# Kernel optimization log

Measured on AMD Instinct MI355X. Metric: run time of the kernel, lower is better.

## Reference

```python
import jax, jax.numpy as jnp
import numpy as np

B, S, D, H = 4, 2048, 1024, 16
HD = D // H


def setup_inputs() -> dict:
    key = jax.random.key(0)
    k1, k2, k3 = jax.random.split(key, 3)
    scale = 1.0 / np.sqrt(D)
    return {
        "x": jax.random.normal(k1, (B, S, D), dtype=jnp.float32),
        "w_qkv": jax.random.normal(k2, (D, 3 * D), dtype=jnp.float32) * scale,
        "b_qkv": jnp.zeros((3 * D,), dtype=jnp.float32),
        "w_out": jax.random.normal(k3, (D, D), dtype=jnp.float32) * scale,
        "b_out": jnp.zeros((D,), dtype=jnp.float32),
    }


def reference(x, w_qkv, b_qkv, w_out, b_out):
    bsz, seqlen, embed = x.shape
    n_head = H
    head_dim = embed // n_head
    att_scale = 1.0 / np.sqrt(head_dim)

    qkv = x @ w_qkv + b_qkv                       # [b, s, 3d]
    q, k, v = jnp.split(qkv, 3, axis=2)
    # [b, h, s, hd]
    q = q.reshape(bsz, seqlen, n_head, head_dim).transpose(0, 2, 1, 3)
    k = k.reshape(bsz, seqlen, n_head, head_dim).transpose(0, 2, 1, 3)
    v = v.reshape(bsz, seqlen, n_head, head_dim).transpose(0, 2, 1, 3)

    att = jnp.einsum("bhqd,bhkd->bhqk", q, k) * att_scale
    causal = jnp.tril(jnp.ones((seqlen, seqlen), dtype=bool))
    att = jnp.where(causal, att, -jnp.inf)
    att = jax.nn.softmax(att, axis=-1)

    y = jnp.einsum("bhqk,bhkd->bhqd", att, v)     # [b, h, s, hd]
    y = y.transpose(0, 2, 1, 3).reshape(bsz, seqlen, embed)
    return y @ w_out + b_out
```

## Files before the change

kernel.cpp:

```cpp
#include <hip/hip_runtime.h>
#include <hip/hip_bf16.h>
#include <cmath>
#include <cstdint>

#define BB 4
#define SS 2048
#define DD 1024
#define HH 16
#define MM (BB * SS)

#define ATT_C 0.18033688011112042f

typedef __attribute__((ext_vector_type(8))) __bf16 bf16x8;
typedef __attribute__((ext_vector_type(4))) float f32x4;
typedef __attribute__((ext_vector_type(8))) float f32x8;
typedef __attribute__((ext_vector_type(8))) unsigned short u16x8;
typedef __attribute__((ext_vector_type(2))) unsigned int u32x2;
typedef __attribute__((ext_vector_type(4))) unsigned int u32x4;

typedef const __attribute__((address_space(3))) unsigned short* lds_cp;

__device__ __forceinline__ unsigned short f2bu(float f) {
  __hip_bfloat16 h = __float2bfloat16(f);
  return __builtin_bit_cast(unsigned short, h);
}

__device__ __forceinline__ f32x4 mfma16(bf16x8 a, bf16x8 b, f32x4 c) {
  return __builtin_amdgcn_mfma_f32_16x16x32_bf16(a, b, c, 0, 0, 0);
}

#define GLD16(gp, lp) __builtin_amdgcn_global_load_lds(                     \
    (const __attribute__((address_space(1))) void*)(gp),                    \
    (__attribute__((address_space(3))) void*)(lp), 16, 0, 0)

#define DSR128(dst, ptr, OFFLIT) \
  asm volatile("ds_read_b128 %0, %1 offset:" OFFLIT : "=v"(dst) : "v"(ptr))
#define LGKM(N) do { asm volatile("s_waitcnt lgkmcnt(" #N ")" ::: "memory"); \
                     __builtin_amdgcn_sched_barrier(0); } while (0)
#define VMCNT(N) do { asm volatile("s_waitcnt vmcnt(" #N ")" ::: "memory"); \
                      __builtin_amdgcn_sched_barrier(0); } while (0)

__global__ __launch_bounds__(256) void k_cast_bf16(const float* __restrict__ in,
                                                   unsigned short* __restrict__ out,
                                                   int n) {
  int i = (blockIdx.x * 256 + threadIdx.x) * 8;
  if (i >= n) return;
  f32x8 v = *(const f32x8*)(in + i);
  u16x8 o;
#pragma unroll
  for (int j = 0; j < 8; ++j) o[j] = f2bu(v[j]);
  *(u16x8*)(out + i) = o;
}

__global__ __launch_bounds__(256) void k_transpose_bf16(const float* __restrict__ in,
                                                        unsigned short* __restrict__ out,
                                                        int R, int C,
                                                        float scale, int scale_end) {
  __shared__ float tile[32][33];
  const int c0 = blockIdx.x * 32, r0 = blockIdx.y * 32;
  const int tx = threadIdx.x & 31, ty = threadIdx.x >> 5;
#pragma unroll
  for (int i = ty; i < 32; i += 8)
    tile[i][tx] = in[(size_t)(r0 + i) * C + c0 + tx];
  __syncthreads();
#pragma unroll
  for (int i = ty; i < 32; i += 8) {
    float v = tile[tx][i];
    if (c0 + i < scale_end) v *= scale;
    out[(size_t)(c0 + i) * R + r0 + tx] = f2bu(v);
  }
}

template <int OUT_F32>
__global__ __launch_bounds__(256) void k_gemm_bt(const unsigned short* __restrict__ A,
                                                 const unsigned short* __restrict__ Bt,
                                                 const float* __restrict__ bias,
                                                 void* __restrict__ Cout,
                                                 int M, int N, int K, int bias_scale_end) {
  __shared__ __attribute__((aligned(16))) unsigned short lA[2][128 * 64];
  __shared__ __attribute__((aligned(16))) unsigned short lB[2][128 * 64];
  const int tid = threadIdx.x;
  const int wave = tid >> 6, lane = tid & 63;
  const int g = lane >> 4, c = lane & 15;
  const int wr = wave >> 1, wc = wave & 1;
  const int m0 = blockIdx.y * 128, n0 = blockIdx.x * 128;
  const int srow = lane >> 3;
  const int sch  = ((lane & 7) ^ srow) * 8;

  f32x4 acc[4][4] = {};
  const int nkt = K >> 6;

#define GSTAGE(buf, kt) do {                                                     \
    const int k0s = (kt) * 64;                                                   \
    _Pragma("unroll")                                                            \
    for (int i_ = 0; i_ < 4; ++i_) {                                             \
      const int chunk = i_ * 4 + wave;                                           \
      GLD16(A + (size_t)(m0 + chunk * 8 + srow) * K + k0s + sch,                 \
            &lA[buf][0] + chunk * 512);                                          \
      GLD16(Bt + (size_t)(n0 + chunk * 8 + srow) * K + k0s + sch,                \
            &lB[buf][0] + chunk * 512);                                          \
    }                                                                            \
  } while (0)

  GSTAGE(0, 0);
  GSTAGE(1, 1);
  VMCNT(8);
  __syncthreads();

  int p = 0;
  for (int kt = 0; kt < nkt; ++kt) {
    const int x7 = c & 7;
    const lds_cp a0 = (lds_cp)&lA[p][0] + (wr * 64 + c) * 64 + (g ^ x7) * 8;
    const lds_cp b0 = (lds_cp)&lB[p][0] + (wc * 64 + c) * 64 + (g ^ x7) * 8;
    const lds_cp a1 = (lds_cp)&lA[p][0] + (wr * 64 + c) * 64 + ((g ^ x7) ^ 4) * 8;
    const lds_cp b1 = (lds_cp)&lB[p][0] + (wc * 64 + c) * 64 + ((g ^ x7) ^ 4) * 8;
    u32x4 af0[4], bf0[4], af1[4], bf1[4];
    DSR128(af0[0], a0, "0");    DSR128(af0[1], a0, "2048");
    DSR128(af0[2], a0, "4096"); DSR128(af0[3], a0, "6144");
    DSR128(bf0[0], b0, "0");    DSR128(bf0[1], b0, "2048");
    DSR128(bf0[2], b0, "4096"); DSR128(bf0[3], b0, "6144");
    DSR128(af1[0], a1, "0");    DSR128(af1[1], a1, "2048");
    DSR128(af1[2], a1, "4096"); DSR128(af1[3], a1, "6144");
    DSR128(bf1[0], b1, "0");    DSR128(bf1[1], b1, "2048");
    DSR128(bf1[2], b1, "4096"); DSR128(bf1[3], b1, "6144");

    LGKM(8);
    __builtin_amdgcn_s_setprio(1);
#pragma unroll
    for (int mi = 0; mi < 4; ++mi)
#pragma unroll
      for (int ni = 0; ni < 4; ++ni)
        acc[mi][ni] = mfma16(__builtin_bit_cast(bf16x8, af0[mi]),
                             __builtin_bit_cast(bf16x8, bf0[ni]), acc[mi][ni]);
    __builtin_amdgcn_s_setprio(0);

    LGKM(0);
    __syncthreads();
    if (kt + 2 < nkt) GSTAGE(p, kt + 2);

    __builtin_amdgcn_s_setprio(1);
#pragma unroll
    for (int mi = 0; mi < 4; ++mi)
#pragma unroll
      for (int ni = 0; ni < 4; ++ni)
        acc[mi][ni] = mfma16(__builtin_bit_cast(bf16x8, af1[mi]),
                             __builtin_bit_cast(bf16x8, bf1[ni]), acc[mi][ni]);
    __builtin_amdgcn_s_setprio(0);

    if (kt + 2 < nkt) { VMCNT(8); } else { VMCNT(0); }
    __syncthreads();
    p ^= 1;
  }
#undef GSTAGE

#pragma unroll
  for (int mi = 0; mi < 4; ++mi)
#pragma unroll
    for (int ni = 0; ni < 4; ++ni) {
      const int col = n0 + wc * 64 + ni * 16 + c;
      float bv = bias[col];
      if (col < bias_scale_end) bv *= ATT_C;
#pragma unroll
      for (int r = 0; r < 4; ++r) {
        const int row = m0 + wr * 64 + mi * 16 + g * 4 + r;
        const float v = acc[mi][ni][r] + bv;
        if (OUT_F32)
          ((float*)Cout)[(size_t)row * N + col] = v;
        else
          ((unsigned short*)Cout)[(size_t)row * N + col] = f2bu(v);
      }
    }
}

__global__ __launch_bounds__(256) void k_attn(const unsigned short* __restrict__ qkv,
                                              unsigned short* __restrict__ y) {
  __shared__ __attribute__((aligned(16))) unsigned short lK[2][4096];
  __shared__ __attribute__((aligned(16))) unsigned short lV[2][4096];

  const int tid = threadIdx.x, wave = tid >> 6, lane = tid & 63;
  const int g = lane >> 4, c = lane & 15;
  const int id = (int)blockIdx.x;
  const int xcd = id & 7, slot = id >> 3;
  const int bh = xcd + 8 * (slot & 7);
  const int pr = slot >> 3;
  const int b = bh >> 4, hc = bh & 15;
  const size_t rb = (size_t)b * SS;

  const int kRow = lane >> 3;
  const int kCh  = ((lane & 7) ^ kRow) * 8;
  const int vRow = 4 * ((lane >> 5) & 1) + ((lane >> 1) & 3);
  const int vDim = 16 * ((lane >> 3) & 3) + (lane & 1) * 8;

#define STAGE(buf, kb) do {                                                        \
    const int k0s = (kb) * 64;                                                     \
    const int g16 = wave * 16;                                                     \
    GLD16(qkv + (rb + k0s + g16 + kRow) * 3072 + 1024 + hc * 64 + kCh,             \
          &lK[buf][0] + g16 * 64);                                                 \
    GLD16(qkv + (rb + k0s + g16 + 8 + kRow) * 3072 + 1024 + hc * 64 + kCh,         \
          &lK[buf][0] + (g16 + 8) * 64);                                           \
    GLD16(qkv + (rb + k0s + g16 + vRow) * 3072 + 2048 + hc * 64 + vDim,            \
          &lV[buf][0] + g16 * 64);                                                 \
    GLD16(qkv + (rb + k0s + g16 + 8 + vRow) * 3072 + 2048 + hc * 64 + vDim,        \
          &lV[buf][0] + (g16 + 8) * 64);                                           \
  } while (0)

#define TRRD(dst, OFFLIT) \
  asm volatile("ds_read_b64_tr_b16 %0, %1 offset:" OFFLIT : "=v"(dst) : "v"(vp))

  bf16x8 onesf;
  {
    u16x8 t;
#pragma unroll
    for (int j = 0; j < 8; ++j) t[j] = 0x3F80;
    onesf = __builtin_bit_cast(bf16x8, t);
  }

  auto run_qtile = [&](int qt) {
    const int qw = qt * 128 + wave * 32;

    bf16x8 qf[2][2];
#pragma unroll
    for (int m = 0; m < 2; ++m)
#pragma unroll
      for (int kh = 0; kh < 2; ++kh)
        qf[m][kh] = *(const bf16x8*)(qkv + (rb + qw + m * 16 + c) * 3072 + hc * 64 + kh * 32 + g * 8);

    float mrun[2] = {-INFINITY, -INFINITY};
    f32x4 lsum[2] = {};
    f32x4 o[2][4] = {};
    const int nkb = 2 * qt + 2;

    auto compute = [&](int buf, int kb) {
      const int k0 = kb * 64;
      if (k0 > qw + 31) return;

      const lds_cp kbase = (lds_cp)&lK[buf][0];
      const lds_cp kp0 = kbase + c * 64 + ((g ^ (c & 7))) * 8;
      const lds_cp kp1 = kbase + c * 64 + (((4 + g) ^ (c & 7))) * 8;
      u32x4 kr[8];
      DSR128(kr[0], kp0, "0");    DSR128(kr[1], kp0, "2048");
      DSR128(kr[2], kp0, "4096"); DSR128(kr[3], kp0, "6144");
      DSR128(kr[4], kp1, "0");    DSR128(kr[5], kp1, "2048");
      DSR128(kr[6], kp1, "4096"); DSR128(kr[7], kp1, "6144");
      const lds_cp vp = (lds_cp)&lV[buf][0] + (lane >> 4) * 256 + (lane & 15) * 4;
      u32x2 t0[8];
      TRRD(t0[0], "0");   TRRD(t0[1], "2048");
      TRRD(t0[2], "128"); TRRD(t0[3], "2176");
      TRRD(t0[4], "256"); TRRD(t0[5], "2304");
      TRRD(t0[6], "384"); TRRD(t0[7], "2432");
      LGKM(8);

      f32x4 s[2][4];
      __builtin_amdgcn_s_setprio(1);
#pragma unroll
      for (int kf = 0; kf < 4; ++kf) {
        const bf16x8 ka = __builtin_bit_cast(bf16x8, kr[kf]);
        const bf16x8 kb2 = __builtin_bit_cast(bf16x8, kr[4 + kf]);
#pragma unroll
        for (int m = 0; m < 2; ++m) {
          f32x4 a = {};
          a = mfma16(ka, qf[m][0], a);
          a = mfma16(kb2, qf[m][1], a);
          s[m][kf] = a;
        }
      }
      __builtin_amdgcn_s_setprio(0);

      u32x2 t1[8];
      TRRD(t1[0], "4096"); TRRD(t1[1], "6144");
      TRRD(t1[2], "4224"); TRRD(t1[3], "6272");
      TRRD(t1[4], "4352"); TRRD(t1[5], "6400");
      TRRD(t1[6], "4480"); TRRD(t1[7], "6528");

#pragma unroll
      for (int m = 0; m < 2; ++m)
#pragma unroll
        for (int kf = 0; kf < 4; ++kf)
          if (k0 + kf * 16 + 15 > qw + m * 16) {
#pragma unroll
            for (int r = 0; r < 4; ++r)
              if (k0 + kf * 16 + 4 * g + r > qw + m * 16 + c) s[m][kf][r] = -INFINITY;
          }

#pragma unroll
      for (int m = 0; m < 2; ++m) {
        float a0 = fmaxf(fmaxf(s[m][0][0], s[m][0][1]), s[m][0][2]);
        float a1 = fmaxf(fmaxf(s[m][0][3], s[m][1][0]), s[m][1][1]);
        float a2 = fmaxf(fmaxf(s[m][1][2], s[m][1][3]), s[m][2][0]);
        float a3 = fmaxf(fmaxf(s[m][2][1], s[m][2][2]), s[m][2][3]);
        float a4 = fmaxf(fmaxf(s[m][3][0], s[m][3][1]), s[m][3][2]);
        float b0 = fmaxf(fmaxf(a0, a1), a2);
        float b1 = fmaxf(fmaxf(a3, a4), s[m][3][3]);
        float tmax = fmaxf(b0, b1);
        tmax = fmaxf(tmax, __shfl_xor(tmax, 16));
        tmax = fmaxf(tmax, __shfl_xor(tmax, 32));
        const float mold = mrun[m];
        float mt;
        if (__all(tmax - mold <= 8.f)) {
          mt = mold;
        } else {
          mt = fmaxf(mold, tmax);
          const float alpha = __builtin_amdgcn_exp2f(mold - mt);
          mrun[m] = mt;
#pragma unroll
          for (int r = 0; r < 4; ++r) {
            const float ao = __shfl(alpha, (lane & 48) + ((lane & 48) >> 2) + r);
            lsum[m][r] *= ao;
#pragma unroll
            for (int dc = 0; dc < 4; ++dc) o[m][dc][r] *= ao;
          }
        }
#pragma unroll
        for (int kf = 0; kf < 4; ++kf)
#pragma unroll
          for (int r = 0; r < 4; ++r)
            s[m][kf][r] = __builtin_amdgcn_exp2f(s[m][kf][r] - mt);
      }

      bf16x8 pa[2][2];
#pragma unroll
      for (int m = 0; m < 2; ++m)
#pragma unroll
        for (int kh = 0; kh < 2; ++kh) {
          u16x8 t;
#pragma unroll
          for (int j = 0; j < 4; ++j) {
            t[j]     = f2bu(s[m][2 * kh][j]);
            t[4 + j] = f2bu(s[m][2 * kh + 1][j]);
          }
          pa[m][kh] = __builtin_bit_cast(bf16x8, t);
        }

      LGKM(8);
      __builtin_amdgcn_s_setprio(1);
#pragma unroll
      for (int m = 0; m < 2; ++m) {
        lsum[m] = mfma16(pa[m][0], onesf, lsum[m]);
        lsum[m] = mfma16(pa[m][1], onesf, lsum[m]);
      }
#pragma unroll
      for (int dc = 0; dc < 4; ++dc) {
        u32x4 vv = {t0[2 * dc][0], t0[2 * dc][1], t0[2 * dc + 1][0], t0[2 * dc + 1][1]};
        const bf16x8 vf = __builtin_bit_cast(bf16x8, vv);
#pragma unroll
        for (int m = 0; m < 2; ++m) o[m][dc] = mfma16(pa[m][0], vf, o[m][dc]);
      }
      __builtin_amdgcn_s_setprio(0);

      LGKM(0);
      __builtin_amdgcn_s_setprio(1);
#pragma unroll
      for (int dc = 0; dc < 4; ++dc) {
        u32x4 vv = {t1[2 * dc][0], t1[2 * dc][1], t1[2 * dc + 1][0], t1[2 * dc + 1][1]};
        const bf16x8 vf = __builtin_bit_cast(bf16x8, vv);
#pragma unroll
        for (int m = 0; m < 2; ++m) o[m][dc] = mfma16(pa[m][1], vf, o[m][dc]);
      }
      __builtin_amdgcn_s_setprio(0);
    };

    __syncthreads();
    STAGE(0, 0);
    asm volatile("s_waitcnt vmcnt(0)" ::: "memory");
    __syncthreads();
    int cur = 0;
    for (int kb = 0; kb < nkb - 1; ++kb) {
      STAGE(cur ^ 1, kb + 1);
      compute(cur, kb);
      asm volatile("s_waitcnt vmcnt(0)" ::: "memory");
      __syncthreads();
      cur ^= 1;
    }
    compute(cur, nkb - 1);

#pragma unroll
    for (int m = 0; m < 2; ++m)
#pragma unroll
      for (int r = 0; r < 4; ++r) {
        const float inv = __builtin_amdgcn_rcpf(lsum[m][r]);
        const int q = qw + m * 16 + 4 * g + r;
#pragma unroll
        for (int dc = 0; dc < 4; ++dc)
          y[(rb + q) * 1024 + hc * 64 + dc * 16 + c] = f2bu(o[m][dc][r] * inv);
      }
  };

  run_qtile(15 - pr);
  run_qtile(pr);
#undef STAGE
#undef TRRD
}

extern "C" void kernel_launch(void* const* d_in, const int* in_sizes, int n_in,
                              void* d_out, int out_size, void* d_ws, size_t ws_size,
                              hipStream_t stream) {
  (void)in_sizes; (void)n_in; (void)out_size; (void)ws_size;
  const float* x     = (const float*)d_in[0];
  const float* w_qkv = (const float*)d_in[1];
  const float* b_qkv = (const float*)d_in[2];
  const float* w_out = (const float*)d_in[3];
  const float* b_out = (const float*)d_in[4];
  float* out = (float*)d_out;

  char* ws = (char*)d_ws;
  unsigned short* x_bf  = (unsigned short*)(ws);
  unsigned short* wqkvT = (unsigned short*)(ws + (size_t)16 * 1048576);
  unsigned short* woutT = (unsigned short*)(ws + (size_t)22 * 1048576);
  unsigned short* qkv   = (unsigned short*)(ws + (size_t)24 * 1048576);

  k_cast_bf16<<<dim3((MM * DD) / (256 * 8)), 256, 0, stream>>>(x, x_bf, MM * DD);
  k_transpose_bf16<<<dim3(3 * DD / 32, DD / 32), 256, 0, stream>>>(w_qkv, wqkvT, DD, 3 * DD,
                                                                   ATT_C, DD);
  k_transpose_bf16<<<dim3(DD / 32, DD / 32), 256, 0, stream>>>(w_out, woutT, DD, DD, 1.f, 0);

  k_gemm_bt<0><<<dim3(3 * DD / 128, MM / 128), 256, 0, stream>>>(
      x_bf, wqkvT, b_qkv, qkv, MM, 3 * DD, DD, DD);

  k_attn<<<dim3(512), 256, 0, stream>>>(qkv, x_bf);

  k_gemm_bt<1><<<dim3(DD / 128, MM / 128), 256, 0, stream>>>(
      x_bf, woutT, b_out, out, MM, DD, DD, 0);
}
```

Before: 173.3 us.

## Use 256x192 tile GEMM with 8 waves for QKV projection

```diff
diff --git a/kernel.cpp b/kernel.cpp
--- a/kernel.cpp
+++ b/kernel.cpp
@@ -39,6 +39,7 @@
                      __builtin_amdgcn_sched_barrier(0); } while (0)
 #define VMCNT(N) do { asm volatile("s_waitcnt vmcnt(" #N ")" ::: "memory"); \
                       __builtin_amdgcn_sched_barrier(0); } while (0)
+#define RBAR() __builtin_amdgcn_s_barrier()
 
 __global__ __launch_bounds__(256) void k_cast_bf16(const float* __restrict__ in,
                                                    unsigned short* __restrict__ out,
@@ -68,6 +69,127 @@
     float v = tile[tx][i];
     if (c0 + i < scale_end) v *= scale;
     out[(size_t)(c0 + i) * R + r0 + tx] = f2bu(v);
+  }
+}
+
+__global__ __launch_bounds__(512, 2) void k_gemm256(const unsigned short* __restrict__ A,
+                                                    const unsigned short* __restrict__ Bt,
+                                                    const float* __restrict__ bias,
+                                                    unsigned short* __restrict__ C,
+                                                    int M, int N, int K, int bse) {
+  __shared__ __attribute__((aligned(16))) unsigned short lA[2][256 * 64];
+  __shared__ __attribute__((aligned(16))) unsigned short lB[2][192 * 64];
+  const int tid = threadIdx.x;
+  const int wave = tid >> 6, lane = tid & 63;
+  const int g = lane >> 4, c = lane & 15;
+  const int wr = wave >> 2, wc = wave & 3;
+  const int m0 = blockIdx.y * 256, n0 = blockIdx.x * 192;
+  const int srow8 = tid >> 3;
+  const int sch = ((tid & 7) ^ (srow8 & 7)) * 8;
+
+  f32x4 acc[8][3] = {};
+  const int nkt = K >> 6;
+
+#define GST(buf, kt) do {                                                    \
+    const int k0s = (kt) * 64;                                               \
+    _Pragma("unroll")                                                        \
+    for (int j_ = 0; j_ < 4; ++j_)                                           \
+      GLD16(A + (size_t)(m0 + j_ * 64 + srow8) * K + k0s + sch,              \
+            &lA[buf][0] + (j_ * 64 + wave * 8) * 64);                        \
+    _Pragma("unroll")                                                        \
+    for (int j_ = 0; j_ < 3; ++j_)                                           \
+      GLD16(Bt + (size_t)(n0 + j_ * 64 + srow8) * K + k0s + sch,             \
+            &lB[buf][0] + (j_ * 64 + wave * 8) * 64);                        \
+  } while (0)
+
+  GST(0, 0);
+
+  for (int kt = 0; kt < nkt; ++kt) {
+    const int p = kt & 1;
+    if (kt + 1 < nkt) {
+      GST(p ^ 1, kt + 1);
+      VMCNT(7);
+    } else {
+      VMCNT(0);
+    }
+    RBAR();
+
+    const lds_cp ap = (lds_cp)&lA[p][0] + (wr * 128 + c) * 64;
+    const lds_cp bp = (lds_cp)&lB[p][0] + (wc * 48 + c) * 64;
+    const int x7 = c & 7;
+    const lds_cp ap0 = ap + (g ^ x7) * 8, ap1 = ap + ((4 + g) ^ x7) * 8;
+    const lds_cp bp0 = bp + (g ^ x7) * 8, bp1 = bp + ((4 + g) ^ x7) * 8;
+    u32x4 af[4], bf[3];
+
+    DSR128(af[0], ap0, "0");    DSR128(af[1], ap0, "2048");
+    DSR128(af[2], ap0, "4096"); DSR128(af[3], ap0, "6144");
+    DSR128(bf[0], bp0, "0");    DSR128(bf[1], bp0, "2048");  DSR128(bf[2], bp0, "4096");
+    RBAR(); LGKM(0);
+    __builtin_amdgcn_s_setprio(1);
+#pragma unroll
+    for (int mi = 0; mi < 4; ++mi)
+#pragma unroll
+      for (int ni = 0; ni < 3; ++ni)
+        acc[mi][ni] = mfma16(__builtin_bit_cast(bf16x8, af[mi]),
+                             __builtin_bit_cast(bf16x8, bf[ni]), acc[mi][ni]);
+    __builtin_amdgcn_s_setprio(0);
+    RBAR();
+
+    DSR128(af[0], ap0, "8192");  DSR128(af[1], ap0, "10240");
+    DSR128(af[2], ap0, "12288"); DSR128(af[3], ap0, "14336");
+    RBAR(); LGKM(0);
+    __builtin_amdgcn_s_setprio(1);
+#pragma unroll
+    for (int mi = 0; mi < 4; ++mi)
+#pragma unroll
+      for (int ni = 0; ni < 3; ++ni)
+        acc[4 + mi][ni] = mfma16(__builtin_bit_cast(bf16x8, af[mi]),
+                                 __builtin_bit_cast(bf16x8, bf[ni]), acc[4 + mi][ni]);
+    __builtin_amdgcn_s_setprio(0);
+    RBAR();
+
+    DSR128(af[0], ap1, "0");    DSR128(af[1], ap1, "2048");
+    DSR128(af[2], ap1, "4096"); DSR128(af[3], ap1, "6144");
+    DSR128(bf[0], bp1, "0");    DSR128(bf[1], bp1, "2048");  DSR128(bf[2], bp1, "4096");
+    RBAR(); LGKM(0);
+    __builtin_amdgcn_s_setprio(1);
+#pragma unroll
+    for (int mi = 0; mi < 4; ++mi)
+#pragma unroll
+      for (int ni = 0; ni < 3; ++ni)
+        acc[mi][ni] = mfma16(__builtin_bit_cast(bf16x8, af[mi]),
+                             __builtin_bit_cast(bf16x8, bf[ni]), acc[mi][ni]);
+    __builtin_amdgcn_s_setprio(0);
+    RBAR();
+
+    DSR128(af[0], ap1, "8192");  DSR128(af[1], ap1, "10240");
+    DSR128(af[2], ap1, "12288"); DSR128(af[3], ap1, "14336");
+    RBAR(); LGKM(0);
+    __builtin_amdgcn_s_setprio(1);
+#pragma unroll
+    for (int mi = 0; mi < 4; ++mi)
+#pragma unroll
+      for (int ni = 0; ni < 3; ++ni)
+        acc[4 + mi][ni] = mfma16(__builtin_bit_cast(bf16x8, af[mi]),
+                                 __builtin_bit_cast(bf16x8, bf[ni]), acc[4 + mi][ni]);
+    __builtin_amdgcn_s_setprio(0);
+    RBAR();
+  }
+#undef GST
+
+#pragma unroll
+  for (int ni = 0; ni < 3; ++ni) {
+    const int col = n0 + wc * 48 + ni * 16 + c;
+    float bv = bias[col];
+    if (col < bse) bv *= ATT_C;
+#pragma unroll
+    for (int mi = 0; mi < 8; ++mi) {
+#pragma unroll
+      for (int r = 0; r < 4; ++r) {
+        const int row = m0 + wr * 128 + mi * 16 + g * 4 + r;
+        C[(size_t)row * N + col] = f2bu(acc[mi][ni][r] + bv);
+      }
+    }
   }
 }
 
@@ -413,7 +535,7 @@
                                                                    ATT_C, DD);
   k_transpose_bf16<<<dim3(DD / 32, DD / 32), 256, 0, stream>>>(w_out, woutT, DD, DD, 1.f, 0);
 
-  k_gemm_bt<0><<<dim3(3 * DD / 128, MM / 128), 256, 0, stream>>>(
+  k_gemm256<<<dim3(3 * DD / 192, MM / 256), 512, 0, stream>>>(
       x_bf, wqkvT, b_qkv, qkv, MM, 3 * DD, DD, DD);
 
   k_attn<<<dim3(512), 256, 0, stream>>>(qkv, x_bf);
```

New measurement: 175.4 us. No clear change (+1.2%).

## Split attention KV loop across two wave groups and merge partial softmax states

Applied to the files above, without the earlier changes.

```diff
diff --git a/kernel.cpp b/kernel.cpp
--- a/kernel.cpp
+++ b/kernel.cpp
@@ -172,12 +172,12 @@
     }
 }
 
-__global__ __launch_bounds__(256) void k_attn(const unsigned short* __restrict__ qkv,
+__global__ __launch_bounds__(512) void k_attn(const unsigned short* __restrict__ qkv,
                                               unsigned short* __restrict__ y) {
-  __shared__ __attribute__((aligned(16))) unsigned short lK[2][4096];
-  __shared__ __attribute__((aligned(16))) unsigned short lV[2][4096];
+  __shared__ __attribute__((aligned(16))) unsigned short smem[32768];
 
   const int tid = threadIdx.x, wave = tid >> 6, lane = tid & 63;
+  const int grp = wave >> 2, gw = wave & 3;
   const int g = lane >> 4, c = lane & 15;
   const int id = (int)blockIdx.x;
   const int xcd = id & 7, slot = id >> 3;
@@ -191,17 +191,22 @@
   const int vRow = 4 * ((lane >> 5) & 1) + ((lane >> 1) & 3);
   const int vDim = 16 * ((lane >> 3) & 3) + (lane & 1) * 8;
 
-#define STAGE(buf, kb) do {                                                        \
+#define KBASE(par) (&smem[0] + (grp * 2 + (par)) * 4096)
+#define VBASE(par) (&smem[16384] + (grp * 2 + (par)) * 4096)
+
+#define STAGE(par, kb) do {                                                        \
     const int k0s = (kb) * 64;                                                     \
-    const int g16 = wave * 16;                                                     \
+    const int g16 = gw * 16;                                                       \
+    unsigned short* kb_ = KBASE(par);                                              \
+    unsigned short* vb_ = VBASE(par);                                              \
     GLD16(qkv + (rb + k0s + g16 + kRow) * 3072 + 1024 + hc * 64 + kCh,             \
-          &lK[buf][0] + g16 * 64);                                                 \
+          kb_ + g16 * 64);                                                         \
     GLD16(qkv + (rb + k0s + g16 + 8 + kRow) * 3072 + 1024 + hc * 64 + kCh,         \
-          &lK[buf][0] + (g16 + 8) * 64);                                           \
+          kb_ + (g16 + 8) * 64);                                                   \
     GLD16(qkv + (rb + k0s + g16 + vRow) * 3072 + 2048 + hc * 64 + vDim,            \
-          &lV[buf][0] + g16 * 64);                                                 \
+          vb_ + g16 * 64);                                                         \
     GLD16(qkv + (rb + k0s + g16 + 8 + vRow) * 3072 + 2048 + hc * 64 + vDim,        \
-          &lV[buf][0] + (g16 + 8) * 64);                                           \
+          vb_ + (g16 + 8) * 64);                                                   \
   } while (0)
 
 #define TRRD(dst, OFFLIT) \
@@ -215,8 +220,10 @@
     onesf = __builtin_bit_cast(bf16x8, t);
   }
 
+  auto rowsel = [&](int r) { return (lane & 48) + ((lane & 48) >> 2) + r; };
+
   auto run_qtile = [&](int qt) {
-    const int qw = qt * 128 + wave * 32;
+    const int qw = qt * 128 + gw * 32;
 
     bf16x8 qf[2][2];
 #pragma unroll
@@ -229,12 +236,13 @@
     f32x4 lsum[2] = {};
     f32x4 o[2][4] = {};
     const int nkb = 2 * qt + 2;
-
-    auto compute = [&](int buf, int kb) {
+    const int steps = qt + 1;
+
+    auto compute = [&](int par, int kb) {
       const int k0 = kb * 64;
       if (k0 > qw + 31) return;
 
-      const lds_cp kbase = (lds_cp)&lK[buf][0];
+      const lds_cp kbase = (lds_cp)KBASE(par);
       const lds_cp kp0 = kbase + c * 64 + ((g ^ (c & 7))) * 8;
       const lds_cp kp1 = kbase + c * 64 + (((4 + g) ^ (c & 7))) * 8;
       u32x4 kr[8];
@@ -242,7 +250,7 @@
       DSR128(kr[2], kp0, "4096"); DSR128(kr[3], kp0, "6144");
       DSR128(kr[4], kp1, "0");    DSR128(kr[5], kp1, "2048");
       DSR128(kr[6], kp1, "4096"); DSR128(kr[7], kp1, "6144");
-      const lds_cp vp = (lds_cp)&lV[buf][0] + (lane >> 4) * 256 + (lane & 15) * 4;
+      const lds_cp vp = (lds_cp)VBASE(par) + (lane >> 4) * 256 + (lane & 15) * 4;
       u32x2 t0[8];
       TRRD(t0[0], "0");   TRRD(t0[1], "2048");
       TRRD(t0[2], "128"); TRRD(t0[3], "2176");
@@ -304,7 +312,7 @@
           mrun[m] = mt;
 #pragma unroll
           for (int r = 0; r < 4; ++r) {
-            const float ao = __shfl(alpha, (lane & 48) + ((lane & 48) >> 2) + r);
+            const float ao = __shfl(alpha, rowsel(r));
             lsum[m][r] *= ao;
 #pragma unroll
             for (int dc = 0; dc < 4; ++dc) o[m][dc][r] *= ao;
@@ -360,35 +368,67 @@
     };
 
     __syncthreads();
-    STAGE(0, 0);
+    STAGE(0, grp);
     asm volatile("s_waitcnt vmcnt(0)" ::: "memory");
     __syncthreads();
-    int cur = 0;
-    for (int kb = 0; kb < nkb - 1; ++kb) {
-      STAGE(cur ^ 1, kb + 1);
-      compute(cur, kb);
+    for (int t = 0; t < steps; ++t) {
+      const int kbn = 2 * (t + 1) + grp;
+      if (kbn < nkb) STAGE((t + 1) & 1, kbn);
+      compute(t & 1, 2 * t + grp);
       asm volatile("s_waitcnt vmcnt(0)" ::: "memory");
       __syncthreads();
-      cur ^= 1;
     }
-    compute(cur, nkb - 1);
-
-#pragma unroll
-    for (int m = 0; m < 2; ++m)
+
+    float* scr = (float*)smem;
+    {
+      const int mw = 1 - grp;
+      scr[0 * 512 + tid] = mrun[mw];
+#pragma unroll
+      for (int r = 0; r < 4; ++r) scr[(1 + r) * 512 + tid] = lsum[mw][r];
+#pragma unroll
+      for (int dc = 0; dc < 4; ++dc)
+#pragma unroll
+        for (int r = 0; r < 4; ++r) scr[(5 + dc * 4 + r) * 512 + tid] = o[mw][dc][r];
+    }
+    __syncthreads();
+    {
+      const int mo = grp;
+      const int ptid = tid ^ 256;
+      const float mA = mrun[mo];
+      const float mB = scr[0 * 512 + ptid];
+      const float mm = fmaxf(mA, mB);
+      const float aA = __builtin_amdgcn_exp2f(mA - mm);
+      const float aB = __builtin_amdgcn_exp2f(mB - mm);
+      float pl[4];
+      f32x4 po[4];
+#pragma unroll
+      for (int r = 0; r < 4; ++r) pl[r] = scr[(1 + r) * 512 + ptid];
+#pragma unroll
+      for (int dc = 0; dc < 4; ++dc)
+#pragma unroll
+        for (int r = 0; r < 4; ++r) po[dc][r] = scr[(5 + dc * 4 + r) * 512 + ptid];
 #pragma unroll
       for (int r = 0; r < 4; ++r) {
-        const float inv = __builtin_amdgcn_rcpf(lsum[m][r]);
-        const int q = qw + m * 16 + 4 * g + r;
-#pragma unroll
-        for (int dc = 0; dc < 4; ++dc)
-          y[(rb + q) * 1024 + hc * 64 + dc * 16 + c] = f2bu(o[m][dc][r] * inv);
-      }
+        const float aAr = __shfl(aA, rowsel(r));
+        const float aBr = __shfl(aB, rowsel(r));
+        const float lt = aAr * lsum[mo][r] + aBr * pl[r];
+        const float inv = __builtin_amdgcn_rcpf(lt);
+        const int q = qw + mo * 16 + 4 * g + r;
+#pragma unroll
+        for (int dc = 0; dc < 4; ++dc) {
+          const float val = aAr * o[mo][dc][r] + aBr * po[dc][r];
+          y[(rb + q) * 1024 + hc * 64 + dc * 16 + c] = f2bu(val * inv);
+        }
+      }
+    }
   };
 
   run_qtile(15 - pr);
   run_qtile(pr);
 #undef STAGE
 #undef TRRD
+#undef KBASE
+#undef VBASE
 }
 
 extern "C" void kernel_launch(void* const* d_in, const int* in_sizes, int n_in,
@@ -416,7 +456,7 @@
   k_gemm_bt<0><<<dim3(3 * DD / 128, MM / 128), 256, 0, stream>>>(
       x_bf, wqkvT, b_qkv, qkv, MM, 3 * DD, DD, DD);
 
-  k_attn<<<dim3(512), 256, 0, stream>>>(qkv, x_bf);
+  k_attn<<<dim3(512), 512, 0, stream>>>(qkv, x_bf);
 
   k_gemm_bt<1><<<dim3(DD / 128, MM / 128), 256, 0, stream>>>(
       x_bf, woutT, b_out, out, MM, DD, DD, 0);
```

After: 200.2 us. +15.5%, slower.

## Use 256x256-tile 8-wave ping-pong GEMM for QKV projection

Applied to the files above, without the earlier changes.

```diff
diff --git a/kernel.cpp b/kernel.cpp
--- a/kernel.cpp
+++ b/kernel.cpp
@@ -39,6 +39,7 @@
                      __builtin_amdgcn_sched_barrier(0); } while (0)
 #define VMCNT(N) do { asm volatile("s_waitcnt vmcnt(" #N ")" ::: "memory"); \
                       __builtin_amdgcn_sched_barrier(0); } while (0)
+#define RBAR() __builtin_amdgcn_s_barrier()
 
 __global__ __launch_bounds__(256) void k_cast_bf16(const float* __restrict__ in,
                                                    unsigned short* __restrict__ out,
@@ -69,6 +70,119 @@
     if (c0 + i < scale_end) v *= scale;
     out[(size_t)(c0 + i) * R + r0 + tx] = f2bu(v);
   }
+}
+
+__global__ __launch_bounds__(512) void k_gemm8p(const unsigned short* __restrict__ A,
+                                                const unsigned short* __restrict__ Bt,
+                                                const float* __restrict__ bias,
+                                                unsigned short* __restrict__ C,
+                                                int M, int N, int K, int bse) {
+  __shared__ __attribute__((aligned(16))) unsigned short lA[2][2][8192];
+  __shared__ __attribute__((aligned(16))) unsigned short lB[2][2][8192];
+  const int tid = threadIdx.x;
+  const int wave = tid >> 6, lane = tid & 63;
+  const int g = lane >> 4, c = lane & 15;
+  const int wr = wave >> 2, wc = wave & 3;
+  const int m0 = blockIdx.y * 256, n0 = blockIdx.x * 256;
+  const int srow = lane >> 3;
+  const int sch  = ((lane & 7) ^ srow) * 8;
+  const int x7 = c & 7;
+
+  f32x4 acc[8][4] = {};
+  const int nkt = K >> 6;
+
+#define STH(half_base, Mat, row0, kt) do {                                        \
+    GLD16(Mat + (size_t)((row0) + wave * 8 + srow) * K + (kt) * 64 + sch,         \
+          (half_base) + wave * 512);                                              \
+    GLD16(Mat + (size_t)((row0) + 64 + wave * 8 + srow) * K + (kt) * 64 + sch,    \
+          (half_base) + 4096 + wave * 512);                                       \
+  } while (0)
+#define STA(d, h, kt) STH(&lA[d][h][0], A,  m0 + (h) * 128, kt)
+#define STB(d, h, kt) STH(&lB[d][h][0], Bt, n0 + (h) * 128, kt)
+
+  const lds_cp pA00 = (lds_cp)&lA[0][wr][0] + c * 64 + ((g ^ x7)) * 8;
+  const lds_cp pA01 = (lds_cp)&lA[0][wr][0] + c * 64 + ((g ^ x7) ^ 4) * 8;
+  const lds_cp pA10 = (lds_cp)&lA[1][wr][0] + c * 64 + ((g ^ x7)) * 8;
+  const lds_cp pA11 = (lds_cp)&lA[1][wr][0] + c * 64 + ((g ^ x7) ^ 4) * 8;
+  const lds_cp pB00 = (lds_cp)&lB[0][wc >> 1][0] + ((wc & 1) * 64 + c) * 64 + ((g ^ x7)) * 8;
+  const lds_cp pB01 = (lds_cp)&lB[0][wc >> 1][0] + ((wc & 1) * 64 + c) * 64 + ((g ^ x7) ^ 4) * 8;
+  const lds_cp pB10 = (lds_cp)&lB[1][wc >> 1][0] + ((wc & 1) * 64 + c) * 64 + ((g ^ x7)) * 8;
+  const lds_cp pB11 = (lds_cp)&lB[1][wc >> 1][0] + ((wc & 1) * 64 + c) * 64 + ((g ^ x7) ^ 4) * 8;
+
+  u32x4 af[4], bfr[4];
+
+#define RDA0(P) do { DSR128(af[0], P, "0");    DSR128(af[1], P, "2048");   \
+                     DSR128(af[2], P, "4096"); DSR128(af[3], P, "6144"); } while (0)
+#define RDA1(P) do { DSR128(af[0], P, "8192");  DSR128(af[1], P, "10240"); \
+                     DSR128(af[2], P, "12288"); DSR128(af[3], P, "14336"); } while (0)
+#define RDB(P)  do { DSR128(bfr[0], P, "0");    DSR128(bfr[1], P, "2048"); \
+                     DSR128(bfr[2], P, "4096"); DSR128(bfr[3], P, "6144"); } while (0)
+#define MF16(mg) do { __builtin_amdgcn_s_setprio(1);                               \
+    _Pragma("unroll") for (int mi = 0; mi < 4; ++mi)                               \
+    _Pragma("unroll") for (int ni = 0; ni < 4; ++ni)                               \
+      acc[(mg) * 4 + mi][ni] = mfma16(__builtin_bit_cast(bf16x8, af[mi]),          \
+                                      __builtin_bit_cast(bf16x8, bfr[ni]),         \
+                                      acc[(mg) * 4 + mi][ni]);                     \
+    __builtin_amdgcn_s_setprio(0); } while (0)
+
+  STA(0, 0, 0); STA(0, 1, 0); STB(0, 0, 0); STB(0, 1, 0);
+  STB(1, 0, 1);
+  VMCNT(2);
+  RBAR();
+
+  for (int it = 0; it < (nkt >> 1); ++it) {
+    const int t1 = 2 * it + 1, t2 = 2 * it + 2, t3 = 2 * it + 3;
+    STB(1, 1, t1);
+    RDA0(pA00); RDB(pB00);
+    RBAR(); LGKM(0); MF16(0); RBAR();
+    STA(1, 0, t1);
+    RDA1(pA00);
+    RBAR(); LGKM(0); MF16(1); RBAR();
+    STA(1, 1, t1);
+    RDA0(pA01); RDB(pB01);
+    RBAR(); LGKM(0); MF16(0); RBAR();
+    if (t2 < nkt) STB(0, 0, t2);
+    RDA1(pA01);
+    RBAR(); LGKM(0); MF16(1);
+    if (t2 < nkt) { VMCNT(2); } else { VMCNT(0); }
+    RBAR();
+    if (t2 < nkt) STB(0, 1, t2);
+    RDA0(pA10); RDB(pB10);
+    RBAR(); LGKM(0); MF16(0); RBAR();
+    if (t2 < nkt) STA(0, 0, t2);
+    RDA1(pA10);
+    RBAR(); LGKM(0); MF16(1); RBAR();
+    if (t2 < nkt) STA(0, 1, t2);
+    RDA0(pA11); RDB(pB11);
+    RBAR(); LGKM(0); MF16(0); RBAR();
+    if (t3 < nkt) STB(1, 0, t3);
+    RDA1(pA11);
+    RBAR(); LGKM(0); MF16(1);
+    VMCNT(2);
+    RBAR();
+  }
+#undef STH
+#undef STA
+#undef STB
+#undef RDA0
+#undef RDA1
+#undef RDB
+#undef MF16
+
+#pragma unroll
+  for (int mi = 0; mi < 8; ++mi)
+#pragma unroll
+    for (int ni = 0; ni < 4; ++ni) {
+      const int col = n0 + wc * 64 + ni * 16 + c;
+      float bv = bias[col];
+      if (col < bse) bv *= ATT_C;
+#pragma unroll
+      for (int r = 0; r < 4; ++r) {
+        const int row = m0 + wr * 128 + mi * 16 + g * 4 + r;
+        C[(size_t)row * N + col] = f2bu(acc[mi][ni][r] + bv);
+      }
+    }
+  (void)M;
 }
 
 template <int OUT_F32>
@@ -413,7 +527,7 @@
                                                                    ATT_C, DD);
   k_transpose_bf16<<<dim3(DD / 32, DD / 32), 256, 0, stream>>>(w_out, woutT, DD, DD, 1.f, 0);
 
-  k_gemm_bt<0><<<dim3(3 * DD / 128, MM / 128), 256, 0, stream>>>(
+  k_gemm8p<<<dim3(3 * DD / 256, MM / 256), 512, 0, stream>>>(
       x_bf, wqkvT, b_qkv, qkv, MM, 3 * DD, DD, DD);
 
   k_attn<<<dim3(512), 256, 0, stream>>>(qkv, x_bf);
```

New measurement: 177.4 us. 2.4% more time.
